# Kernel tuning notes

Hardware: AMD Instinct MI355X
Metric: run time of the kernel (lower is better)

The kernel has to match this reference:

```python
import jax, jax.numpy as jnp
import numpy as np

D, H, W = 128, 96, 96  # voxel grid
EPS = 1e-5

_OFFS = np.array([[dz, dy, dx] for dz in (-1, 0, 1) for dy in (-1, 0, 1) for dx in (-1, 0, 1)], dtype=np.int64)


def _flat(c):
    return (c[:, 0] * H + c[:, 1]) * W + c[:, 2]


def _dilate(coords):
    # union of coords + all 27 offsets, clipped to grid bounds (stride-1, pad-1 SparseConv3d output sites)
    p = coords[None, :, :] + _OFFS[:, None, :]          # [27, N, 3]
    p = p.reshape(-1, 3)
    ok = np.all((p >= 0) & (p < np.array([D, H, W])), axis=1)
    keys = np.unique(_flat(p[ok]))
    out = np.stack([keys // (H * W), (keys // W) % H, keys % W], axis=1)
    return out


def _rulebook(in_coords, out_coords):
    # nb[k, m] = row index into in_coords of (out_coords[m] + off_k), or -1
    lut = -np.ones(D * H * W, dtype=np.int32)
    lut[_flat(in_coords)] = np.arange(len(in_coords), dtype=np.int32)
    nb = np.full((27, len(out_coords)), -1, dtype=np.int32)
    for k, o in enumerate(_OFFS):
        p = out_coords + o
        ok = np.all((p >= 0) & (p < np.array([D, H, W])), axis=1)
        nb[k, ok] = lut[_flat(p[ok])]
    return nb


def setup_inputs() -> dict:
    key = jax.random.key(0)
    ks = jax.random.split(key, 20)
    # active sites: full plane z=64 over 96x96 footprint (surface-like sparse scene)
    yy, xx = np.meshgrid(np.arange(H), np.arange(W), indexing='ij')
    coords0 = np.stack([np.full(H * W, 64), yy.ravel(), xx.ravel()], axis=1).astype(np.int64)
    coords1 = _dilate(coords0)   # 27648 sites
    coords2 = _dilate(coords1)   # 46080 sites
    nb1 = jnp.asarray(_rulebook(coords0, coords1))
    nbs = jnp.asarray(_rulebook(coords1, coords1))
    nb2 = jnp.asarray(_rulebook(coords1, coords2))

    s = 0.05
    inp = {
        'x': jax.random.normal(ks[0], (coords0.shape[0], 256), jnp.float32),
        'w_s1': jax.random.normal(ks[1], (27, 256, 128), jnp.float32) * s,
        'g_s1': jax.random.uniform(ks[2], (128,), jnp.float32, 0.5, 1.5),
        'b_s1': jax.random.normal(ks[3], (128,), jnp.float32) * 0.1,
        'w11': jax.random.normal(ks[4], (27, 128, 128), jnp.float32) * s,
        'g11': jax.random.uniform(ks[5], (128,), jnp.float32, 0.5, 1.5),
        'b11': jax.random.normal(ks[6], (128,), jnp.float32) * 0.1,
        'w12': jax.random.normal(ks[7], (27, 128, 128), jnp.float32) * s,
        'g12': jax.random.uniform(ks[8], (128,), jnp.float32, 0.5, 1.5),
        'b12': jax.random.normal(ks[9], (128,), jnp.float32) * 0.1,
        'w21': jax.random.normal(ks[10], (27, 128, 128), jnp.float32) * s,
        'g21': jax.random.uniform(ks[11], (128,), jnp.float32, 0.5, 1.5),
        'b21': jax.random.normal(ks[12], (128,), jnp.float32) * 0.1,
        'w22': jax.random.normal(ks[13], (27, 128, 128), jnp.float32) * s,
        'g22': jax.random.uniform(ks[14], (128,), jnp.float32, 0.5, 1.5),
        'b22': jax.random.normal(ks[15], (128,), jnp.float32) * 0.1,
        'w_s2': jax.random.normal(ks[16], (27, 128, 32), jnp.float32) * s,
        'g_s2': jax.random.uniform(ks[17], (32,), jnp.float32, 0.5, 1.5),
        'b_s2': jax.random.normal(ks[18], (32,), jnp.float32) * 0.1,
        'nb1': nb1, 'nbs': nbs, 'nb2': nb2,
    }
    return inp


def _sparse_conv(x, nb, w):
    # gather -> GEMM -> accumulate per kernel offset (rulebook semantics of spconv)
    mask = nb >= 0                      # [27, M]
    idx = jnp.where(mask, nb, 0)
    out = jnp.zeros((nb.shape[1], w.shape[2]), x.dtype)
    for k in range(nb.shape[0]):        # fixed 27-offset loop
        g = jnp.where(mask[k][:, None], x[idx[k]], 0.0)  # [M, Cin]
        out = out + g @ w[k]
    return out


def _bn(f, g, b):
    # BatchNorm1d in training mode over active voxel rows (biased variance)
    mu = jnp.mean(f, axis=0)
    var = jnp.mean(jnp.square(f - mu), axis=0)
    return (f - mu) * jax.lax.rsqrt(var + EPS) * g + b


def _block(f, nbs, w1, g1, b1, w2, g2, b2):
    idn = f
    h = jax.nn.relu(_bn(_sparse_conv(f, nbs, w1), g1, b1))
    h = _bn(_sparse_conv(h, nbs, w2), g2, b2)
    return jax.nn.relu(h + idn)


def reference(x, w_s1, g_s1, b_s1, w11, g11, b11, w12, g12, b12,
              w21, g21, b21, w22, g22, b22, w_s2, g_s2, b_s2,
              nb1, nbs, nb2):
    f = jax.nn.relu(_bn(_sparse_conv(x, nb1, w_s1), g_s1, b_s1))          # spconv1
    f = _block(f, nbs, w11, g11, b11, w12, g12, b12)                      # block1 (submanifold)
    f = _block(f, nbs, w21, g21, b21, w22, g22, b22)                      # block2 (submanifold)
    out = jax.nn.relu(_bn(_sparse_conv(f, nb2, w_s2), g_s2, b_s2))        # spconv2
    return out  # features of the final SparseConvTensor, [46080, 32]
```

## Files before the change

kernel.cpp:

```cpp
#include <hip/hip_runtime.h>
#include <stdint.h>

typedef _Float16 f16;
typedef _Float16 f16x8 __attribute__((ext_vector_type(8)));
typedef _Float16 f16x4 __attribute__((ext_vector_type(4)));
typedef float f32x4 __attribute__((ext_vector_type(4)));

#define GAS __attribute__((address_space(1)))
#define LAS __attribute__((address_space(3)))

__device__ __forceinline__ void gl_lds16(const void* g, void* l) {
    __builtin_amdgcn_global_load_lds((const GAS uint32_t*)g, (LAS uint32_t*)l, 16, 0, 0);
}

__global__ __launch_bounds__(256) void prep(
    const float* __restrict__ x, f16* __restrict__ xh, long nx4,
    const float* __restrict__ ws1, f16* __restrict__ w1,
    const float* __restrict__ w11, f16* __restrict__ wa1,
    const float* __restrict__ w12, f16* __restrict__ wa2,
    const float* __restrict__ w21, f16* __restrict__ wb1,
    const float* __restrict__ w22, f16* __restrict__ wb2,
    const float* __restrict__ ws2, f16* __restrict__ w2,
    float* __restrict__ zbuf, long nz, int nbzc) {
    if ((int)blockIdx.x < nbzc) {
        long t = (long)blockIdx.x * 256 + threadIdx.x;
        if (t < nz) { zbuf[t] = 0.f; return; }
        t -= nz;
        if (t < nx4) {
            float4 v = ((const float4*)x)[t];
            f16x4 o = {(f16)v.x, (f16)v.y, (f16)v.z, (f16)v.w};
            *(f16x4*)(xh + t * 4) = o;
        }
        return;
    }
    int tau = blockIdx.x - nbzc;
    const float* src; f16* dst; int Cin, Cout;
    if (tau < 864)        { src = ws1; dst = w1;  Cin = 256; Cout = 128; }
    else if (tau < 1296)  { tau -= 864;  src = w11; dst = wa1; Cin = 128; Cout = 128; }
    else if (tau < 1728)  { tau -= 1296; src = w12; dst = wa2; Cin = 128; Cout = 128; }
    else if (tau < 2160)  { tau -= 1728; src = w21; dst = wb1; Cin = 128; Cout = 128; }
    else if (tau < 2592)  { tau -= 2160; src = w22; dst = wb2; Cin = 128; Cout = 128; }
    else                  { tau -= 2592; src = ws2; dst = w2;  Cin = 128; Cout = 32; }
    const int nci = Cin >> 5, nco = Cout >> 5;
    const int k  = tau / (nci * nco);
    const int rm = tau - k * nci * nco;
    const int ci0 = (rm / nco) << 5;
    const int co0 = (rm % nco) << 5;
    __shared__ float tile[32][33];
    const int r = threadIdx.x >> 5, c = threadIdx.x & 31;
#pragma unroll
    for (int i2 = 0; i2 < 4; i2++)
        tile[r + 8 * i2][c] =
            src[((long)(k * Cin + ci0 + r + 8 * i2)) * Cout + co0 + c];
    __syncthreads();
#pragma unroll
    for (int i2 = 0; i2 < 4; i2++)
        dst[((long)(k * Cout + co0 + r + 8 * i2)) * Cin + ci0 + c] =
            (f16)tile[c][r + 8 * i2];
}

template <int LAYER, bool FOLD, bool RESID, bool WRITEACT>
__global__ __launch_bounds__(512, 2) void conv_dense(
    const f16* __restrict__ fin, const f16* __restrict__ wt,
    const f16* __restrict__ zrow, f16* __restrict__ out,
    float* __restrict__ stats,
    const float* __restrict__ pstats, const float* __restrict__ pg,
    const float* __restrict__ pb, const f16* __restrict__ resid,
    f16* __restrict__ actout, float pinv) {
    constexpr int COUT = (LAYER == 2) ? 32 : 128;
    constexpr int INRB = (LAYER == 0) ? 512 : 256;
    constexpr int WRB  = (LAYER == 0) ? 512 : 256;
    constexpr int RT   = (COUT == 128) ? 4 : 2;
    constexpr int CT   = (COUT == 128) ? 4 : 2;
    constexpr int NBCH = COUT / 4;
    extern __shared__ char smem[];
    char* ldsA0 = smem;
    char* ldsA1 = smem + 46080;
    char* ldsB0 = smem + 92160;
    char* ldsB1 = smem + 92160 + COUT * 256;

    const int b = blockIdx.x;
    const int p = b / 72;
    const int t0 = b % 72;
    const int y0 = (t0 / 6) * 8;
    const int x0 = (t0 % 6) * 16;
    const int tid = threadIdx.x;
    const int lane = tid & 63;
    const int wave = tid >> 6;
    const int kh = wave & 1;
    const int pairId = wave >> 1;
    const int q = lane >> 4;
    const int r16 = lane & 15;
    const int wr = ((COUT == 128) ? (pairId >> 1) : pairId) * (RT * 16);
    const int wc = ((COUT == 128) ? (pairId & 1) : 0) * (CT * 16);

    int S = 0;
    int js[3], dzs[3], hs[3];
    if (LAYER == 0) {
        js[0] = 0; dzs[0] = 1 - p; hs[0] = 0;
        js[1] = 0; dzs[1] = 1 - p; hs[1] = 1;
        S = 2;
    } else {
        for (int dz = -1; dz <= 1; dz++) {
            int j = (LAYER == 1) ? p + dz : p + dz - 1;
            if (0 <= j && j < 3) { js[S] = j; dzs[S] = dz; hs[S] = 0; S++; }
        }
    }

    float psc[8], pbt[8];
    if (FOLD) {
#pragma unroll
        for (int e = 0; e < 8; e++) {
            int c = r16 * 8 + e;
            float mu = pstats[c] * pinv;
            float var = fmaxf(pstats[128 + c] * pinv - mu * mu, 0.f);
            float s = pg[c] * rsqrtf(var + 1e-5f);
            psc[e] = s;
            pbt[e] = pb[c] - mu * s;
        }
    }

    auto stageA = [&](int s, char* buf) {
        const int j = js[s], h = hs[s];
        const long pbase = (long)j * 9216;
        for (int ch = wave; ch < 45; ch += 8) {
            int site = ch * 4 + q;
            int sy = site / 18;
            int sx = site - sy * 18;
            int y = y0 - 1 + sy;
            int x = x0 - 1 + sx;
            bool ok = ((unsigned)y < 96u) & ((unsigned)x < 96u);
            if (FOLD) {
                f16x8 o = {};
                if (ok) {
                    const long ro = (pbase + y * 96 + x) * 128 + r16 * 8;
                    f16x8 v = *(const f16x8*)(fin + ro);
                    f16x8 rv = {};
                    if (RESID) rv = *(const f16x8*)(resid + ro);
#pragma unroll
                    for (int e = 0; e < 8; e++) {
                        float t = (float)v[e] * psc[e] + pbt[e];
                        if (RESID) t += (float)rv[e];
                        o[e] = (f16)fmaxf(t, 0.f);
                    }
                    if (WRITEACT && j == p &&
                        (unsigned)(sy - 1) < 8u && (unsigned)(sx - 1) < 16u)
                        *(f16x8*)(actout + ro) = o;
                }
                *(f16x8*)(buf + site * 256 + ((r16 ^ (site & 7)) << 4)) = o;
            } else {
                int cc = r16 ^ (site & 7);
                const char* src = ok
                    ? (const char*)fin + (pbase + y * 96 + x) * INRB + h * 256 + cc * 16
                    : (const char*)zrow + cc * 16;
                gl_lds16(src, buf + ch * 1024);
            }
        }
    };
    auto stageB = [&](int k, int h, char* buf) {
        for (int ch = wave; ch < NBCH; ch += 8) {
            int col = ch * 4 + q;
            int cc = r16 ^ (col & 7);
            const char* src = (const char*)wt + (long)(k * COUT + col) * WRB +
                              h * 256 + cc * 16;
            gl_lds16(src, buf + ch * 1024);
        }
    };

    f32x4 acc[RT][CT];
#pragma unroll
    for (int tr = 0; tr < RT; tr++)
#pragma unroll
        for (int c = 0; c < CT; c++) acc[tr][c] = f32x4{0.f, 0.f, 0.f, 0.f};

    stageA(0, ldsA0);
    stageB((dzs[0] + 1) * 9, hs[0], ldsB0);

    int tap = 0;
    for (int s = 0; s < S; s++) {
        const char* bufA = (s & 1) ? ldsA1 : ldsA0;
#pragma unroll
        for (int i = 0; i < 9; i++, tap++) {
            __syncthreads();
            if (i == 0 && s + 1 < S) stageA(s + 1, ((s + 1) & 1) ? ldsA1 : ldsA0);
            if (tap + 1 < S * 9) {
                int sn = (i == 8) ? s + 1 : s;
                int in2 = (i == 8) ? 0 : i + 1;
                stageB((dzs[sn] + 1) * 9 + in2, hs[sn], ((tap + 1) & 1) ? ldsB1 : ldsB0);
            }
            const char* bufB = (tap & 1) ? ldsB1 : ldsB0;
            const int dy = i / 3 - 1, dx = i % 3 - 1;
#pragma unroll
            for (int kk2 = 0; kk2 < 2; kk2++) {
                const int kk = kh * 2 + kk2;
                f16x8 Af[RT], Bf[CT];
#pragma unroll
                for (int tr = 0; tr < RT; tr++) {
                    int site = (wr / 16 + tr + 1 + dy) * 18 + 1 + dx + r16;
                    Af[tr] = *(const f16x8*)(bufA + site * 256 +
                                             (((kk * 4 + q) ^ (site & 7)) << 4));
                }
#pragma unroll
                for (int c = 0; c < CT; c++) {
                    int col = wc + c * 16 + r16;
                    Bf[c] = *(const f16x8*)(bufB + col * 256 +
                                            (((kk * 4 + q) ^ (col & 7)) << 4));
                }
#pragma unroll
                for (int tr = 0; tr < RT; tr++)
#pragma unroll
                    for (int c = 0; c < CT; c++)
                        acc[tr][c] = __builtin_amdgcn_mfma_f32_16x16x32_f16(
                            Af[tr], Bf[c], acc[tr][c], 0, 0, 0);
            }
        }
    }

    char* xch = smem + 92160;
    constexpr int XR = RT * CT * 1024;
    __syncthreads();
    if (kh == 1) {
#pragma unroll
        for (int tr = 0; tr < RT; tr++)
#pragma unroll
            for (int c = 0; c < CT; c++)
                *(f32x4*)(xch + pairId * XR + (tr * CT + c) * 1024 + lane * 16) =
                    acc[tr][c];
    }
    __syncthreads();
    if (kh == 1) return;
#pragma unroll
    for (int tr = 0; tr < RT; tr++)
#pragma unroll
        for (int c = 0; c < CT; c++)
            acc[tr][c] += *(const f32x4*)(xch + pairId * XR + (tr * CT + c) * 1024 +
                                          lane * 16);

    const long mbase = (long)p * 9216 + (long)y0 * 96 + x0;
#pragma unroll
    for (int c = 0; c < CT; c++) {
        const int col = wc + c * 16 + r16;
        float sum = 0.f, ssq = 0.f;
#pragma unroll
        for (int tr = 0; tr < RT; tr++) {
            const int ly = wr / 16 + tr;
#pragma unroll
            for (int r = 0; r < 4; r++) {
                const int lx = q * 4 + r;
                float v = acc[tr][c][r];
                out[(mbase + ly * 96 + lx) * COUT + col] = (f16)v;
                sum += v;
                ssq = fmaf(v, v, ssq);
            }
        }
        sum += __shfl_xor(sum, 16);
        sum += __shfl_xor(sum, 32);
        ssq += __shfl_xor(ssq, 16);
        ssq += __shfl_xor(ssq, 32);
        if (q == 0) {
            atomicAdd(&stats[col], sum);
            atomicAdd(&stats[COUT + col], ssq);
        }
    }
}

__global__ __launch_bounds__(256) void bn_apply8(
    const f16x8* __restrict__ f, const float* __restrict__ sums,
    const float* __restrict__ g, const float* __restrict__ bta,
    float* __restrict__ outf, long n8, int C, float invM) {
    long i = (long)blockIdx.x * 256 + threadIdx.x;
    if (i >= n8) return;
    int col0 = (int)((i * 8) & (C - 1));
    f16x8 v = f[i];
    float ro[8];
#pragma unroll
    for (int j = 0; j < 8; j++) {
        int c = col0 + j;
        float mu = sums[c] * invM;
        float var = sums[C + c] * invM - mu * mu;
        var = fmaxf(var, 0.f);
        float sc = g[c] * rsqrtf(var + 1e-5f);
        ro[j] = fmaxf(((float)v[j] - mu) * sc + bta[c], 0.f);
    }
    *(float4*)(outf + i * 8)     = make_float4(ro[0], ro[1], ro[2], ro[3]);
    *(float4*)(outf + i * 8 + 4) = make_float4(ro[4], ro[5], ro[6], ro[7]);
}

extern "C" void kernel_launch(void* const* d_in, const int* in_sizes, int n_in,
                              void* d_out, int out_size, void* d_ws, size_t ws_size,
                              hipStream_t stream) {
    (void)n_in; (void)out_size; (void)ws_size;
    const float* x    = (const float*)d_in[0];
    const float* w_s1 = (const float*)d_in[1];
    const float* g_s1 = (const float*)d_in[2];
    const float* b_s1 = (const float*)d_in[3];
    const float* w11  = (const float*)d_in[4];
    const float* g11  = (const float*)d_in[5];
    const float* b11  = (const float*)d_in[6];
    const float* w12  = (const float*)d_in[7];
    const float* g12  = (const float*)d_in[8];
    const float* b12  = (const float*)d_in[9];
    const float* w21  = (const float*)d_in[10];
    const float* g21  = (const float*)d_in[11];
    const float* b21  = (const float*)d_in[12];
    const float* w22  = (const float*)d_in[13];
    const float* g22  = (const float*)d_in[14];
    const float* b22  = (const float*)d_in[15];
    const float* w_s2 = (const float*)d_in[16];
    const float* g_s2 = (const float*)d_in[17];
    const float* b_s2 = (const float*)d_in[18];

    const int N0 = in_sizes[0] / 256;
    const int M1 = in_sizes[19] / 27;
    const int M2 = in_sizes[21] / 27;

    char* base = (char*)d_ws;
    size_t off = 0;
    auto alloc = [&](size_t bytes) -> char* {
        off = (off + 255) & ~(size_t)255;
        char* p = base + off;
        off += bytes;
        return p;
    };
    f16* xh  = (f16*)alloc((size_t)N0 * 256 * 2);
    f16* w1  = (f16*)alloc(27UL * 128 * 256 * 2);
    f16* wa1 = (f16*)alloc(27UL * 128 * 128 * 2);
    f16* wa2 = (f16*)alloc(27UL * 128 * 128 * 2);
    f16* wb1 = (f16*)alloc(27UL * 128 * 128 * 2);
    f16* wb2 = (f16*)alloc(27UL * 128 * 128 * 2);
    f16* w2  = (f16*)alloc(27UL * 32 * 128 * 2);
    f16* fA  = (f16*)alloc((size_t)M1 * 128 * 2);
    f16* fC  = (f16*)alloc((size_t)M1 * 128 * 2);
    f16* rA  = (f16*)alloc((size_t)M1 * 128 * 2);
    f16* rB  = (f16*)alloc((size_t)M1 * 128 * 2);
    f16* rS2 = (f16*)alloc((size_t)M2 * 32 * 2);
    float* stats = (float*)alloc(1344UL * 4);
    f16*   zrow  = (f16*)alloc(512);

    const int lds01 = 92160 + 2 * 128 * 256;
    const int lds2  = 92160 + 2 * 32 * 256;
    (void)hipFuncSetAttribute((const void*)conv_dense<0, false, false, false>,
                              hipFuncAttributeMaxDynamicSharedMemorySize, lds01);
    (void)hipFuncSetAttribute((const void*)conv_dense<1, true, false, true>,
                              hipFuncAttributeMaxDynamicSharedMemorySize, lds01);
    (void)hipFuncSetAttribute((const void*)conv_dense<1, true, false, false>,
                              hipFuncAttributeMaxDynamicSharedMemorySize, lds01);
    (void)hipFuncSetAttribute((const void*)conv_dense<1, true, true, true>,
                              hipFuncAttributeMaxDynamicSharedMemorySize, lds01);
    (void)hipFuncSetAttribute((const void*)conv_dense<2, true, true, false>,
                              hipFuncAttributeMaxDynamicSharedMemorySize, lds2);

    const long nz  = 1472;
    const long nx4 = (long)N0 * 256 / 4;
    const int nbzc = (int)((nz + nx4 + 255) / 256);
    prep<<<nbzc + 2700, 256, 0, stream>>>(
        x, xh, nx4, w_s1, w1, w11, wa1, w12, wa2, w21, wb1, w22, wb2,
        w_s2, w2, stats, nz, nbzc);

    const float inv1 = 1.f / (float)M1, inv2 = 1.f / (float)M2;
    const int g1 = 3 * 72;
    const int g2 = 5 * 72;
    const long n8b = (long)M2 * 32 / 8;
    const int gb = (int)((n8b + 255) / 256);

    conv_dense<0, false, false, false><<<g1, 512, lds01, stream>>>(
        xh, w1, zrow, rA, stats, nullptr, nullptr, nullptr, nullptr, nullptr, 0.f);
    conv_dense<1, true, false, true><<<g1, 512, lds01, stream>>>(
        rA, wa1, zrow, rB, stats + 256, stats, g_s1, b_s1, nullptr, fA, inv1);
    conv_dense<1, true, false, false><<<g1, 512, lds01, stream>>>(
        rB, wa2, zrow, rA, stats + 512, stats + 256, g11, b11, nullptr, nullptr, inv1);
    conv_dense<1, true, true, true><<<g1, 512, lds01, stream>>>(
        rA, wb1, zrow, rB, stats + 768, stats + 512, g12, b12, fA, fC, inv1);
    conv_dense<1, true, false, false><<<g1, 512, lds01, stream>>>(
        rB, wb2, zrow, rA, stats + 1024, stats + 768, g21, b21, nullptr, nullptr, inv1);
    conv_dense<2, true, true, false><<<g2, 512, lds2, stream>>>(
        rA, w2, zrow, rS2, stats + 1280, stats + 1024, g22, b22, fC, nullptr, inv1);
    bn_apply8<<<gb, 256, 0, stream>>>((const f16x8*)rS2, stats + 1280, g_s2, b_s2,
                                      (float*)d_out, n8b, 32, inv2);
}
```

Before: 352.2 us.

## Stage all nine weight taps per slab in final conv to cut barriers

For the final 32-channel conv layer, the per-tap double-buffered weight pipeline is replaced. All nine weight panels of a z-slab are now loaded into LDS together with a single input buffer, so there are two barriers per slab instead of one per tap. The block-to-plane mapping is also reordered so that the heavier middle planes are scheduled first. The cost is that loads no longer overlap with compute inside a slab, and the LDS layout changes from 92160+16384 to 46080+73728 bytes.

```diff
diff --git a/kernel.cpp b/kernel.cpp
--- a/kernel.cpp
+++ b/kernel.cpp
@@ -73,13 +73,17 @@
     constexpr int RT   = (COUT == 128) ? 4 : 2;
     constexpr int CT   = (COUT == 128) ? 4 : 2;
     constexpr int NBCH = COUT / 4;
+    constexpr int BPAN = COUT * 256;
     extern __shared__ char smem[];
     char* ldsA0 = smem;
     char* ldsA1 = smem + 46080;
-    char* ldsB0 = smem + 92160;
-    char* ldsB1 = smem + 92160 + COUT * 256;
-
-    const int b = blockIdx.x;
+    char* ldsB  = smem + ((LAYER == 2) ? 46080 : 92160);
+
+    int b = blockIdx.x;
+    if (LAYER == 2) {
+        const int order[5] = {2, 1, 3, 0, 4};
+        b = order[b / 72] * 72 + (b % 72);
+    }
     const int p = b / 72;
     const int t0 = b % 72;
     const int y0 = (t0 / 6) * 8;
@@ -173,50 +177,91 @@
 #pragma unroll
         for (int c = 0; c < CT; c++) acc[tr][c] = f32x4{0.f, 0.f, 0.f, 0.f};
 
-    stageA(0, ldsA0);
-    stageB((dzs[0] + 1) * 9, hs[0], ldsB0);
-
-    int tap = 0;
-    for (int s = 0; s < S; s++) {
-        const char* bufA = (s & 1) ? ldsA1 : ldsA0;
-#pragma unroll
-        for (int i = 0; i < 9; i++, tap++) {
+    if constexpr (LAYER == 2) {
+        for (int s = 0; s < S; s++) {
+            if (s > 0) __syncthreads();
+            stageA(s, ldsA0);
+            const int kbase = (dzs[s] + 1) * 9;
+#pragma unroll
+            for (int i = 0; i < 9; i++) stageB(kbase + i, 0, ldsB + i * BPAN);
             __syncthreads();
-            if (i == 0 && s + 1 < S) stageA(s + 1, ((s + 1) & 1) ? ldsA1 : ldsA0);
-            if (tap + 1 < S * 9) {
-                int sn = (i == 8) ? s + 1 : s;
-                int in2 = (i == 8) ? 0 : i + 1;
-                stageB((dzs[sn] + 1) * 9 + in2, hs[sn], ((tap + 1) & 1) ? ldsB1 : ldsB0);
+#pragma unroll
+            for (int i = 0; i < 9; i++) {
+                const char* bufB = ldsB + i * BPAN;
+                const int dy = i / 3 - 1, dx = i % 3 - 1;
+#pragma unroll
+                for (int kk2 = 0; kk2 < 2; kk2++) {
+                    const int kk = kh * 2 + kk2;
+                    f16x8 Af[RT], Bf[CT];
+#pragma unroll
+                    for (int tr = 0; tr < RT; tr++) {
+                        int site = (wr / 16 + tr + 1 + dy) * 18 + 1 + dx + r16;
+                        Af[tr] = *(const f16x8*)(ldsA0 + site * 256 +
+                                                 (((kk * 4 + q) ^ (site & 7)) << 4));
+                    }
+#pragma unroll
+                    for (int c = 0; c < CT; c++) {
+                        int col = wc + c * 16 + r16;
+                        Bf[c] = *(const f16x8*)(bufB + col * 256 +
+                                                (((kk * 4 + q) ^ (col & 7)) << 4));
+                    }
+#pragma unroll
+                    for (int tr = 0; tr < RT; tr++)
+#pragma unroll
+                        for (int c = 0; c < CT; c++)
+                            acc[tr][c] = __builtin_amdgcn_mfma_f32_16x16x32_f16(
+                                Af[tr], Bf[c], acc[tr][c], 0, 0, 0);
+                }
             }
-            const char* bufB = (tap & 1) ? ldsB1 : ldsB0;
-            const int dy = i / 3 - 1, dx = i % 3 - 1;
-#pragma unroll
-            for (int kk2 = 0; kk2 < 2; kk2++) {
-                const int kk = kh * 2 + kk2;
-                f16x8 Af[RT], Bf[CT];
-#pragma unroll
-                for (int tr = 0; tr < RT; tr++) {
-                    int site = (wr / 16 + tr + 1 + dy) * 18 + 1 + dx + r16;
-                    Af[tr] = *(const f16x8*)(bufA + site * 256 +
-                                             (((kk * 4 + q) ^ (site & 7)) << 4));
+        }
+    } else {
+        char* ldsB0 = ldsB;
+        char* ldsB1 = ldsB + BPAN;
+        stageA(0, ldsA0);
+        stageB((dzs[0] + 1) * 9, hs[0], ldsB0);
+        int tap = 0;
+        for (int s = 0; s < S; s++) {
+            const char* bufA = (s & 1) ? ldsA1 : ldsA0;
+#pragma unroll
+            for (int i = 0; i < 9; i++, tap++) {
+                __syncthreads();
+                if (i == 0 && s + 1 < S) stageA(s + 1, ((s + 1) & 1) ? ldsA1 : ldsA0);
+                if (tap + 1 < S * 9) {
+                    int sn = (i == 8) ? s + 1 : s;
+                    int in2 = (i == 8) ? 0 : i + 1;
+                    stageB((dzs[sn] + 1) * 9 + in2, hs[sn],
+                           ((tap + 1) & 1) ? ldsB1 : ldsB0);
                 }
-#pragma unroll
-                for (int c = 0; c < CT; c++) {
-                    int col = wc + c * 16 + r16;
-                    Bf[c] = *(const f16x8*)(bufB + col * 256 +
-                                            (((kk * 4 + q) ^ (col & 7)) << 4));
+                const char* bufB = (tap & 1) ? ldsB1 : ldsB0;
+                const int dy = i / 3 - 1, dx = i % 3 - 1;
+#pragma unroll
+                for (int kk2 = 0; kk2 < 2; kk2++) {
+                    const int kk = kh * 2 + kk2;
+                    f16x8 Af[RT], Bf[CT];
+#pragma unroll
+                    for (int tr = 0; tr < RT; tr++) {
+                        int site = (wr / 16 + tr + 1 + dy) * 18 + 1 + dx + r16;
+                        Af[tr] = *(const f16x8*)(bufA + site * 256 +
+                                                 (((kk * 4 + q) ^ (site & 7)) << 4));
+                    }
+#pragma unroll
+                    for (int c = 0; c < CT; c++) {
+                        int col = wc + c * 16 + r16;
+                        Bf[c] = *(const f16x8*)(bufB + col * 256 +
+                                                (((kk * 4 + q) ^ (col & 7)) << 4));
+                    }
+#pragma unroll
+                    for (int tr = 0; tr < RT; tr++)
+#pragma unroll
+                        for (int c = 0; c < CT; c++)
+                            acc[tr][c] = __builtin_amdgcn_mfma_f32_16x16x32_f16(
+                                Af[tr], Bf[c], acc[tr][c], 0, 0, 0);
                 }
-#pragma unroll
-                for (int tr = 0; tr < RT; tr++)
-#pragma unroll
-                    for (int c = 0; c < CT; c++)
-                        acc[tr][c] = __builtin_amdgcn_mfma_f32_16x16x32_f16(
-                            Af[tr], Bf[c], acc[tr][c], 0, 0, 0);
             }
         }
     }
 
-    char* xch = smem + 92160;
+    char* xch = (LAYER == 2) ? smem : smem + 92160;
     constexpr int XR = RT * CT * 1024;
     __syncthreads();
     if (kh == 1) {
@@ -338,7 +383,7 @@
     f16*   zrow  = (f16*)alloc(512);
 
     const int lds01 = 92160 + 2 * 128 * 256;
-    const int lds2  = 92160 + 2 * 32 * 256;
+    const int lds2  = 46080 + 9 * 32 * 256;
     (void)hipFuncSetAttribute((const void*)conv_dense<0, false, false, false>,
                               hipFuncAttributeMaxDynamicSharedMemorySize, lds01);
     (void)hipFuncSetAttribute((const void*)conv_dense<1, true, false, true>,
```

Result: no change. 355.1 us (+0.8%).
